# Kernel optimization log

Measured on AMD Instinct MI355X. Metric: run time of the kernel, lower is better.

Reference implementation:

```python
import jax, jax.numpy as jnp
import numpy as np

T_MAX = 20
NUM_HEADS = 8
COMPLEXITY_W = 0.3
LN_EPS = 1e-5


def _layernorm(h, g, b):
    mu = jnp.mean(h, axis=-1, keepdims=True)
    var = jnp.var(h, axis=-1, keepdims=True)
    return (h - mu) / jnp.sqrt(var + LN_EPS) * g + b


def _gate_mlp(x, W1, b1, g, be, W2, b2, W3, b3):
    # Linear -> LayerNorm -> ReLU -> (Dropout=id in eval) -> Linear -> ReLU -> Linear -> Sigmoid
    h = jax.nn.relu(_layernorm(x @ W1 + b1, g, be))
    h = jax.nn.relu(h @ W2 + b2)
    return jax.nn.sigmoid(h @ W3 + b3)


def _adaptive_windows(x, p):
    S = x.shape[1]
    gate = _gate_mlp(x, p['gW1'], p['gb1'], p['gg'], p['gbe'], p['gW2'], p['gb2'], p['gW3'], p['gb3'])
    comp = _gate_mlp(x, p['cW1'], p['cb1'], p['cg'], p['cbe'], p['cW2'], p['cb2'], p['cW3'], p['cb3'])
    pos = jnp.linspace(0.8, 1.2, S, dtype=x.dtype).reshape(1, -1, 1)
    score = ((1.0 - COMPLEXITY_W) * gate + COMPLEXITY_W * comp) * pos
    T_i = jnp.clip(jnp.ceil(score[..., 0] * T_MAX), 1, T_MAX).astype(jnp.int32)  # [B,S]
    return T_i


def _spike_sum(x, T_i, alpha, beta):
    # LIF recurrence over T_MAX steps; accumulate masked spikes. x: [B,S,E]
    z = jnp.zeros_like(x)

    def step(carry, t):
        v, i, acc = carry
        active = (t < T_i).astype(x.dtype)[..., None]  # [B,S,1]
        i = alpha * i + x * active
        v = beta * v + i
        s = (v >= 1.0).astype(x.dtype)
        v = v * (1.0 - s)  # v_reset = 0
        return (v, i, acc + s * active), None

    (_, _, acc), _ = jax.lax.scan(step, (z, z, z), jnp.arange(T_MAX))
    return acc


def _forward(x, params):
    B, S, E = x.shape
    H, D = NUM_HEADS, E // NUM_HEADS
    q = x @ params['Wq']
    k = x @ params['Wk']
    v = x @ params['Wv']
    T_i = _adaptive_windows(x, params)
    q_sum = _spike_sum(q, T_i, params['alpha_q'], params['beta_q'])
    k_sum = _spike_sum(k, T_i, params['alpha_k'], params['beta_k'])
    v_mean = _spike_sum(v, T_i, params['alpha_v'], params['beta_v']) / T_MAX
    q_sum = q_sum.reshape(B, S, H, D)
    k_sum = k_sum.reshape(B, S, H, D)
    v_mean = v_mean.reshape(B, S, H, D)
    scale = D ** -0.5
    scores = jnp.einsum('bihd,bjhd->bhij', q_sum, k_sum) * scale
    w = jax.nn.softmax(scores, axis=-1)
    out = jnp.einsum('bhij,bjhd->bihd', w, v_mean).reshape(B, S, E)
    return out @ params['Wo'] + params['bo']


def setup_inputs() -> dict:
    key = jax.random.key(0)
    ks = iter(jax.random.split(key, 32))
    B, S, E = 4, 1024, 512
    f32 = jnp.float32

    def w(shape, scale=0.02):
        return jax.random.normal(next(ks), shape, dtype=f32) * scale

    inp = {
        'x': jax.random.normal(next(ks), (B, S, E), dtype=f32),
        'Wq': w((E, E)), 'Wk': w((E, E)), 'Wv': w((E, E)),
        'Wo': w((E, E)), 'bo': jnp.zeros((E,), f32),
        'gW1': w((E, 128)), 'gb1': jnp.zeros((128,), f32),
        'gg': jnp.ones((128,), f32), 'gbe': jnp.zeros((128,), f32),
        'gW2': w((128, 64)), 'gb2': jnp.zeros((64,), f32),
        'gW3': w((64, 1)), 'gb3': jnp.zeros((1,), f32),
        'cW1': w((E, 64)), 'cb1': jnp.zeros((64,), f32),
        'cg': jnp.ones((64,), f32), 'cbe': jnp.zeros((64,), f32),
        'cW2': w((64, 32)), 'cb2': jnp.zeros((32,), f32),
        'cW3': w((32, 1)), 'cb3': jnp.zeros((1,), f32),
        'alpha_q': jnp.asarray(np.exp(-1 / 5.0), f32), 'beta_q': jnp.asarray(np.exp(-1 / 20.0), f32),
        'alpha_k': jnp.asarray(np.exp(-1 / 5.0), f32), 'beta_k': jnp.asarray(np.exp(-1 / 20.0), f32),
        'alpha_v': jnp.asarray(np.exp(-1 / 5.0), f32), 'beta_v': jnp.asarray(np.exp(-1 / 20.0), f32),
    }
    return inp


def reference(x, Wq, Wk, Wv, Wo, bo,
              gW1, gb1, gg, gbe, gW2, gb2, gW3, gb3,
              cW1, cb1, cg, cbe, cW2, cb2, cW3, cb3,
              alpha_q, beta_q, alpha_k, beta_k, alpha_v, beta_v):
    params = dict(Wq=Wq, Wk=Wk, Wv=Wv, Wo=Wo, bo=bo,
                  gW1=gW1, gb1=gb1, gg=gg, gbe=gbe, gW2=gW2, gb2=gb2, gW3=gW3, gb3=gb3,
                  cW1=cW1, cb1=cb1, cg=cg, cbe=cbe, cW2=cW2, cb2=cb2, cW3=cW3, cb3=cb3,
                  alpha_q=alpha_q, beta_q=beta_q, alpha_k=alpha_k, beta_k=beta_k,
                  alpha_v=alpha_v, beta_v=beta_v)
    return _forward(x, params)
```

## Files before the change

### kernel.cpp

```cpp
#include <hip/hip_runtime.h>
#include <math.h>

#define SEQ   1024
#define EMB   512
#define NROWS 4096
#define LDP   72
#define GROWS 8
#define LDW   40

typedef __attribute__((ext_vector_type(8))) short short8;
typedef __attribute__((ext_vector_type(4))) float float4v;

__device__ __forceinline__ float bf2f(unsigned short s) {
    union { float f; unsigned u; } x; x.u = ((unsigned)s) << 16; return x.f;
}
__device__ __forceinline__ unsigned short f2bf(float f) {
    union { float f; unsigned u; } x; x.f = f;
    unsigned r = x.u + 0x7fffu + ((x.u >> 16) & 1u);
    return (unsigned short)(r >> 16);
}

__device__ __forceinline__ void split3(float x, unsigned short& h, unsigned short& m, unsigned short& l) {
    union { float f; unsigned u; } a; a.f = x;
    const unsigned rh = a.u + 0x7fffu + ((a.u >> 16) & 1u);
    h = (unsigned short)(rh >> 16);
    union { float f; unsigned u; } hf; hf.u = rh & 0xffff0000u;
    const float r1 = x - hf.f;
    a.f = r1;
    const unsigned rm = a.u + 0x7fffu + ((a.u >> 16) & 1u);
    m = (unsigned short)(rm >> 16);
    union { float f; unsigned u; } mf; mf.u = rm & 0xffff0000u;
    const float r2 = r1 - mf.f;
    l = f2bf(r2);
}

template<int H1, int H2>
__device__ __forceinline__ double gate_mlp_block(
    const double xs[GROWS][EMB], double h1[GROWS][128], double h2[GROWS][64],
    double* mu_s, double* var_s,
    const float* __restrict__ W1, const float* __restrict__ b1,
    const float* __restrict__ gam, const float* __restrict__ bet,
    const float* __restrict__ W2, const float* __restrict__ b2,
    const float* __restrict__ W3, const float* __restrict__ b3,
    int tid, int myrow)
{
    constexpr int RN1 = GROWS * H1 / 256;
    constexpr int RN2 = GROWS * H2 / 256;

    {
        const int col = tid % H1;
        const int rb  = (tid / H1) * RN1;
        double acc[RN1];
        #pragma unroll
        for (int r = 0; r < RN1; ++r) acc[r] = (double)b1[col];
        for (int k = 0; k < EMB; ++k) {
            const double w = (double)W1[k * H1 + col];
            #pragma unroll
            for (int r = 0; r < RN1; ++r) acc[r] += w * xs[rb + r][k];
        }
        #pragma unroll
        for (int r = 0; r < RN1; ++r) h1[rb + r][col] = acc[r];
    }
    __syncthreads();

    {
        const int r = tid >> 5, l = tid & 31;
        double s = 0.0;
        for (int c = l; c < H1; c += 32) s += h1[r][c];
        #pragma unroll
        for (int off = 16; off >= 1; off >>= 1) s += __shfl_xor(s, off);
        if (l == 0) mu_s[r] = s / (double)H1;
    }
    __syncthreads();
    {
        const int r = tid >> 5, l = tid & 31;
        const double mu = mu_s[r];
        double s = 0.0;
        for (int c = l; c < H1; c += 32) { const double d = h1[r][c] - mu; s += d * d; }
        #pragma unroll
        for (int off = 16; off >= 1; off >>= 1) s += __shfl_xor(s, off);
        if (l == 0) var_s[r] = s / (double)H1;
    }
    __syncthreads();
    for (int idx = tid; idx < GROWS * H1; idx += 256) {
        const int r = idx / H1, cc = idx % H1;
        double hn = (h1[r][cc] - mu_s[r]) / sqrt(var_s[r] + 1e-5) * (double)gam[cc] + (double)bet[cc];
        h1[r][cc] = hn > 0.0 ? hn : 0.0;
    }
    __syncthreads();

    {
        const int col = tid % H2;
        const int rb  = (tid / H2) * RN2;
        double acc[RN2];
        #pragma unroll
        for (int r = 0; r < RN2; ++r) acc[r] = (double)b2[col];
        for (int k = 0; k < H1; ++k) {
            const double w = (double)W2[k * H2 + col];
            #pragma unroll
            for (int r = 0; r < RN2; ++r) acc[r] += w * h1[rb + r][k];
        }
        #pragma unroll
        for (int r = 0; r < RN2; ++r) h2[rb + r][col] = acc[r] > 0.0 ? acc[r] : 0.0;
    }
    __syncthreads();

    {
        const int r = tid >> 5, l = tid & 31;
        double s = 0.0;
        for (int c = l; c < H2; c += 32) s += h2[r][c] * (double)W3[c];
        #pragma unroll
        for (int off = 16; off >= 1; off >>= 1) s += __shfl_xor(s, off);
        if (l == 0) mu_s[r] = s;
    }
    __syncthreads();
    double ret = 0.0;
    if (myrow >= 0) {
        const double z = mu_s[myrow] + (double)b3[0];
        ret = 1.0 / (1.0 + exp(-z));
    }
    __syncthreads();
    return ret;
}

__global__ __launch_bounds__(256) void gates_kernel(
    const float* __restrict__ x,
    const float* __restrict__ gW1, const float* __restrict__ gb1,
    const float* __restrict__ gg,  const float* __restrict__ gbe,
    const float* __restrict__ gW2, const float* __restrict__ gb2,
    const float* __restrict__ gW3, const float* __restrict__ gb3,
    const float* __restrict__ cW1, const float* __restrict__ cb1,
    const float* __restrict__ cg,  const float* __restrict__ cbe,
    const float* __restrict__ cW2, const float* __restrict__ cb2,
    const float* __restrict__ cW3, const float* __restrict__ cb3,
    int* __restrict__ T_i)
{
    __shared__ double xs[GROWS][EMB];
    __shared__ double h1[GROWS][128];
    __shared__ double h2[GROWS][64];
    __shared__ double mu_s[GROWS], var_s[GROWS];

    const int row0 = blockIdx.x * GROWS;
    const int tid = threadIdx.x;

    for (int idx = tid; idx < GROWS * EMB; idx += 256) {
        const int r = idx >> 9, cc = idx & 511;
        xs[r][cc] = (double)x[(size_t)(row0 + r) * EMB + cc];
    }
    __syncthreads();

    const int myrow = (tid < GROWS) ? tid : -1;
    const double g0 = gate_mlp_block<128, 64>(xs, h1, h2, mu_s, var_s,
                                              gW1, gb1, gg, gbe, gW2, gb2, gW3, gb3, tid, myrow);
    const double c0 = gate_mlp_block<64, 32>(xs, h1, h2, mu_s, var_s,
                                             cW1, cb1, cg, cbe, cW2, cb2, cW3, cb3, tid, myrow);

    if (tid < GROWS) {
        const int row = row0 + tid;
        const int s = row & (SEQ - 1);
        const double step = (1.2 - 0.8) / (double)(SEQ - 1);
        const double pos  = (double)s * step + 0.8;
        const double score = ((1.0 - 0.3) * g0 + 0.3 * c0) * pos;
        double t = ceil(score * 20.0);
        t = t < 1.0 ? 1.0 : (t > 20.0 ? 20.0 : t);
        T_i[row] = (int)t;
    }
}

__global__ __launch_bounds__(256) void w_limbs_prep(
    const float* __restrict__ Wq, const float* __restrict__ Wk, const float* __restrict__ Wv,
    unsigned short* __restrict__ WL)
{
    const int z = blockIdx.z;
    const float* __restrict__ W = (z == 0) ? Wq : (z == 1) ? Wk : Wv;
    unsigned short* __restrict__ Th = WL + (size_t)z * 3 * EMB * EMB;
    unsigned short* __restrict__ Tm = Th + (size_t)EMB * EMB;
    unsigned short* __restrict__ Tl = Tm + (size_t)EMB * EMB;

    __shared__ __align__(16) float Ws[64][68];
    const int k0 = blockIdx.y * 64, n0 = blockIdx.x * 64;
    const int t = threadIdx.x;
    #pragma unroll
    for (int it = 0; it < 4; ++it) {
        const int idx = it * 256 + t;
        const int r = idx >> 4, c4 = (idx & 15) * 4;
        *(float4*)&Ws[r][c4] = *(const float4*)&W[(size_t)(k0 + r) * EMB + n0 + c4];
    }
    __syncthreads();
    #pragma unroll
    for (int it = 0; it < 2; ++it) {
        const int idx = it * 256 + t;
        const int n = idx >> 3, k8 = (idx & 7) * 8;
        short8 ph, pm, pl;
        #pragma unroll
        for (int j = 0; j < 8; ++j) {
            unsigned short h, m, l;
            split3(Ws[k8 + j][n], h, m, l);
            ph[j] = (short)h; pm[j] = (short)m; pl[j] = (short)l;
        }
        const size_t o = (size_t)(n0 + n) * EMB + k0 + k8;
        *(short8*)&Th[o] = ph;
        *(short8*)&Tm[o] = pm;
        *(short8*)&Tl[o] = pl;
    }
}

__global__ __launch_bounds__(256) void qkv_mfma_lif_kernel(
    const float* __restrict__ x, const unsigned short* __restrict__ WL,
    const float* __restrict__ aq, const float* __restrict__ bq,
    const float* __restrict__ akp, const float* __restrict__ bkp,
    const float* __restrict__ av, const float* __restrict__ bv,
    const int* __restrict__ T_i,
    unsigned short* __restrict__ q_sum, unsigned short* __restrict__ k_sum,
    unsigned short* __restrict__ v_mean)
{
    const int z = blockIdx.z;
    const unsigned short* __restrict__ WTh = WL + (size_t)z * 3 * EMB * EMB;
    const unsigned short* __restrict__ WTm = WTh + (size_t)EMB * EMB;
    const unsigned short* __restrict__ WTl = WTm + (size_t)EMB * EMB;
    unsigned short* __restrict__ out = (z == 0) ? q_sum : (z == 1) ? k_sum : v_mean;
    const double alpha = (double)((z == 0) ? aq : (z == 1) ? akp : av)[0];
    const double beta  = (double)((z == 0) ? bq : (z == 1) ? bkp : bv)[0];

    __shared__ __align__(16) short Ah[128 * LDW], Am2[128 * LDW], Al2[128 * LDW];
    __shared__ __align__(16) short Bh[64 * LDW],  Bm2[64 * LDW],  Bl2[64 * LDW];

    const int tid  = threadIdx.x;
    const int lane = tid & 63, wave = tid >> 6;
    const int qd = lane >> 4, c = lane & 15;
    const int wrow = wave * 32;
    const int row0 = blockIdx.y * 128, col0 = blockIdx.x * 64;

    const int am = tid >> 1, ak = (tid & 1) * 16;
    const int bn = tid >> 2, bk = (tid & 3) * 8;

    float4v acc[2][4];
    #pragma unroll
    for (int i = 0; i < 2; ++i)
        #pragma unroll
        for (int j = 0; j < 4; ++j)
            acc[i][j] = (float4v){0.f, 0.f, 0.f, 0.f};

    for (int k0 = 0; k0 < EMB; k0 += 32) {
        const float* xp = &x[(size_t)(row0 + am) * EMB + k0 + ak];
        const float4 a0 = *(const float4*)(xp + 0);
        const float4 a1 = *(const float4*)(xp + 4);
        const float4 a2 = *(const float4*)(xp + 8);
        const float4 a3 = *(const float4*)(xp + 12);
        const size_t boff = (size_t)(col0 + bn) * EMB + k0 + bk;
        const short8 b8h = *(const short8*)&WTh[boff];
        const short8 b8m = *(const short8*)&WTm[boff];
        const short8 b8l = *(const short8*)&WTl[boff];

        const float av16[16] = {a0.x, a0.y, a0.z, a0.w, a1.x, a1.y, a1.z, a1.w,
                                a2.x, a2.y, a2.z, a2.w, a3.x, a3.y, a3.z, a3.w};
        unsigned short lh[16], lm[16], ll[16];
        #pragma unroll
        for (int e = 0; e < 16; ++e) split3(av16[e], lh[e], lm[e], ll[e]);
        short8 ph0, ph1, pm0, pm1, pl0, pl1;
        #pragma unroll
        for (int e = 0; e < 8; ++e) {
            ph0[e] = (short)lh[e]; ph1[e] = (short)lh[e + 8];
            pm0[e] = (short)lm[e]; pm1[e] = (short)lm[e + 8];
            pl0[e] = (short)ll[e]; pl1[e] = (short)ll[e + 8];
        }

        __syncthreads();
        {
            const int ao = am * LDW + ak;
            *(short8*)&Ah[ao]      = ph0; *(short8*)&Ah[ao + 8]  = ph1;
            *(short8*)&Am2[ao]     = pm0; *(short8*)&Am2[ao + 8] = pm1;
            *(short8*)&Al2[ao]     = pl0; *(short8*)&Al2[ao + 8] = pl1;
            const int bo = bn * LDW + bk;
            *(short8*)&Bh[bo]  = b8h;
            *(short8*)&Bm2[bo] = b8m;
            *(short8*)&Bl2[bo] = b8l;
        }
        __syncthreads();

        short8 Afh[2], Afm[2], Afl[2];
        #pragma unroll
        for (int i = 0; i < 2; ++i) {
            const int ab = (wrow + i * 16 + c) * LDW + qd * 8;
            Afh[i] = *(const short8*)&Ah[ab];
            Afm[i] = *(const short8*)&Am2[ab];
            Afl[i] = *(const short8*)&Al2[ab];
        }
        short8 Bfh[4], Bfm[4], Bfl[4];
        #pragma unroll
        for (int j = 0; j < 4; ++j) {
            const int bb = (j * 16 + c) * LDW + qd * 8;
            Bfh[j] = *(const short8*)&Bh[bb];
            Bfm[j] = *(const short8*)&Bm2[bb];
            Bfl[j] = *(const short8*)&Bl2[bb];
        }

        #pragma unroll
        for (int i = 0; i < 2; ++i)
            #pragma unroll
            for (int j = 0; j < 4; ++j) {
                float4v t = acc[i][j];
                t = __builtin_amdgcn_mfma_f32_16x16x32_bf16(Afh[i], Bfh[j], t, 0, 0, 0);
                t = __builtin_amdgcn_mfma_f32_16x16x32_bf16(Afh[i], Bfm[j], t, 0, 0, 0);
                t = __builtin_amdgcn_mfma_f32_16x16x32_bf16(Afm[i], Bfh[j], t, 0, 0, 0);
                t = __builtin_amdgcn_mfma_f32_16x16x32_bf16(Afm[i], Bfm[j], t, 0, 0, 0);
                t = __builtin_amdgcn_mfma_f32_16x16x32_bf16(Afh[i], Bfl[j], t, 0, 0, 0);
                t = __builtin_amdgcn_mfma_f32_16x16x32_bf16(Afl[i], Bfh[j], t, 0, 0, 0);
                acc[i][j] = t;
            }
    }

    #pragma unroll
    for (int i = 0; i < 2; ++i)
        #pragma unroll
        for (int r = 0; r < 4; ++r) {
            const int gm = row0 + wrow + i * 16 + qd * 4 + r;
            const int T = T_i[gm];
            #pragma unroll
            for (int j = 0; j < 4; ++j) {
                const double xv = (double)acc[i][j][r];
                double cur = 0.0, vm = 0.0, spikes = 0.0;
                for (int t = 0; t < T; ++t) {
                    cur = alpha * cur + xv;
                    vm  = beta * vm + cur;
                    if (vm >= 1.0) { spikes += 1.0; vm = 0.0; }
                }
                if (z == 2) spikes = spikes / 20.0;
                out[(size_t)gm * EMB + col0 + j * 16 + c] = f2bf((float)spikes);
            }
        }
}

__global__ __launch_bounds__(256) void attn_mfma_kernel(
    const unsigned short* __restrict__ q, const unsigned short* __restrict__ k,
    const unsigned short* __restrict__ v, unsigned short* __restrict__ attn_bf)
{
    __shared__ __align__(16) short Ks[64 * LDP];
    __shared__ __align__(16) short Pt[64 * LDP];
    __shared__ __align__(16) short Vt[64 * LDP];

    const int b = blockIdx.z, h = blockIdx.y;
    const int i0 = blockIdx.x * 64;
    const int tid  = threadIdx.x;
    const int wave = tid >> 6, lane = tid & 63;
    const int quad = lane >> 4, c = lane & 15;

    const unsigned short* Qb = q + ((size_t)b * SEQ + i0) * EMB + h * 64;
    const unsigned short* Kb = k + (size_t)b * SEQ * EMB + h * 64;
    const unsigned short* Vb = v + (size_t)b * SEQ * EMB + h * 64;

    short8 qf[2];
    {
        const int qrow = wave * 16 + c;
        #pragma unroll
        for (int ks = 0; ks < 2; ++ks) {
            short8 raw = *(const short8*)(Qb + (size_t)qrow * EMB + ks * 32 + quad * 8);
            short8 sc8;
            #pragma unroll
            for (int j = 0; j < 8; ++j)
                sc8[j] = (short)f2bf(bf2f((unsigned short)raw[j]) * 0.125f);
            qf[ks] = sc8;
        }
    }

    float m_r[4], l_r[4];
    float4v o[4];
    #pragma unroll
    for (int r = 0; r < 4; ++r) { m_r[r] = -1e30f; l_r[r] = 0.f; }
    #pragma unroll
    for (int nb = 0; nb < 4; ++nb)
        #pragma unroll
        for (int r = 0; r < 4; ++r) o[nb][r] = 0.f;

    for (int jt = 0; jt < SEQ / 64; ++jt) {
        #pragma unroll
        for (int it = 0; it < 2; ++it) {
            const int idx = it * 256 + tid;
            const int row = idx >> 3, ch = idx & 7;
            short8 val = *(const short8*)(Kb + (size_t)(jt * 64 + row) * EMB + ch * 8);
            *(short8*)&Ks[row * LDP + ch * 8] = val;
        }
        __syncthreads();

        float sc[4][4];
        #pragma unroll
        for (int nb = 0; nb < 4; ++nb) {
            float4v acc = {0.f, 0.f, 0.f, 0.f};
            #pragma unroll
            for (int ks = 0; ks < 2; ++ks) {
                short8 bfrag = *(const short8*)&Ks[(nb * 16 + c) * LDP + ks * 32 + quad * 8];
                acc = __builtin_amdgcn_mfma_f32_16x16x32_bf16(qf[ks], bfrag, acc, 0, 0, 0);
            }
            #pragma unroll
            for (int r = 0; r < 4; ++r) sc[nb][r] = acc[r];
        }

        float mnew[4], alpha[4];
        #pragma unroll
        for (int r = 0; r < 4; ++r) {
            float mx = fmaxf(fmaxf(sc[0][r], sc[1][r]), fmaxf(sc[2][r], sc[3][r]));
            #pragma unroll
            for (int off = 8; off >= 1; off >>= 1) mx = fmaxf(mx, __shfl_xor(mx, off));
            mnew[r]  = fmaxf(m_r[r], mx);
            alpha[r] = __expf(m_r[r] - mnew[r]);
            m_r[r]   = mnew[r];
        }
        float psum[4] = {0.f, 0.f, 0.f, 0.f};
        #pragma unroll
        for (int nb = 0; nb < 4; ++nb)
            #pragma unroll
            for (int r = 0; r < 4; ++r) {
                float p = __expf(sc[nb][r] - mnew[r]);
                psum[r] += p;
                Pt[(wave * 16 + quad * 4 + r) * LDP + nb * 16 + c] = (short)f2bf(p);
            }
        #pragma unroll
        for (int r = 0; r < 4; ++r) {
            float s = psum[r];
            #pragma unroll
            for (int off = 8; off >= 1; off >>= 1) s += __shfl_xor(s, off);
            l_r[r] = l_r[r] * alpha[r] + s;
            #pragma unroll
            for (int nb = 0; nb < 4; ++nb) o[nb][r] *= alpha[r];
        }

        {
            const int m = tid & 7, rp = tid >> 3;
            const int r = rp * 2;
            short8 v0 = *(const short8*)(Vb + (size_t)(jt * 64 + r) * EMB + m * 8);
            short8 v1 = *(const short8*)(Vb + (size_t)(jt * 64 + r + 1) * EMB + m * 8);
            const int rch = r >> 3, rlow = r & 7;
            #pragma unroll
            for (int i = 0; i < 8; ++i) {
                const int d = m * 8 + i;
                const int col = ((rch ^ m) << 3) + rlow;
                *(int*)&Vt[d * LDP + col] =
                    (int)((unsigned)(unsigned short)v0[i] |
                          ((unsigned)(unsigned short)v1[i] << 16));
            }
        }
        __syncthreads();

        short8 pf[2];
        #pragma unroll
        for (int ks = 0; ks < 2; ++ks)
            pf[ks] = *(const short8*)&Pt[(wave * 16 + c) * LDP + ks * 32 + quad * 8];
        #pragma unroll
        for (int nb = 0; nb < 4; ++nb) {
            float4v acc = o[nb];
            #pragma unroll
            for (int ks = 0; ks < 2; ++ks) {
                const int d = nb * 16 + c;
                const int kch = ks * 4 + quad;
                const int col = ((kch ^ (d >> 3)) << 3);
                short8 vfrag = *(const short8*)&Vt[d * LDP + col];
                acc = __builtin_amdgcn_mfma_f32_16x16x32_bf16(pf[ks], vfrag, acc, 0, 0, 0);
            }
            o[nb] = acc;
        }
    }

    #pragma unroll
    for (int r = 0; r < 4; ++r) {
        const float inv = 1.0f / l_r[r];
        const int row = i0 + wave * 16 + quad * 4 + r;
        #pragma unroll
        for (int nb = 0; nb < 4; ++nb)
            attn_bf[((size_t)b * SEQ + row) * EMB + h * 64 + nb * 16 + c] =
                f2bf(o[nb][r] * inv);
    }
}

__global__ __launch_bounds__(256) void wot_prep(
    const float* __restrict__ Wo, unsigned short* __restrict__ BT)
{
    __shared__ unsigned short Ws[64][72];
    const int k0 = blockIdx.y * 64, n0 = blockIdx.x * 64;
    const int t = threadIdx.x;
    #pragma unroll
    for (int it = 0; it < 4; ++it) {
        const int idx = it * 256 + t;
        const int r = idx >> 4, c4 = (idx & 15) * 4;
        const float4 w4 = *(const float4*)&Wo[(size_t)(k0 + r) * EMB + n0 + c4];
        Ws[r][c4 + 0] = f2bf(w4.x); Ws[r][c4 + 1] = f2bf(w4.y);
        Ws[r][c4 + 2] = f2bf(w4.z); Ws[r][c4 + 3] = f2bf(w4.w);
    }
    __syncthreads();
    #pragma unroll
    for (int it = 0; it < 2; ++it) {
        const int idx = it * 256 + t;
        const int n = idx >> 3, k8 = (idx & 7) * 8;
        short8 pack;
        #pragma unroll
        for (int j = 0; j < 8; ++j) pack[j] = (short)Ws[k8 + j][n];
        *(short8*)&BT[(size_t)(n0 + n) * EMB + k0 + k8] = pack;
    }
}

__global__ __launch_bounds__(256) void out_gemm_kernel(
    const unsigned short* __restrict__ A,
    const unsigned short* __restrict__ BT,
    const float* __restrict__ bias, float* __restrict__ out)
{
    const int tid  = threadIdx.x;
    const int lane = tid & 63, wave = tid >> 6;
    const int qd = lane >> 4, c = lane & 15;
    const int wm = (wave & 1) * 32, wn = (wave >> 1) * 32;
    const int row0 = blockIdx.y * 64, col0 = blockIdx.x * 64;

    float4v acc[2][2];
    #pragma unroll
    for (int i = 0; i < 2; ++i)
        #pragma unroll
        for (int j = 0; j < 2; ++j)
            acc[i][j] = (float4v){0.f, 0.f, 0.f, 0.f};

    for (int k0 = 0; k0 < EMB; k0 += 32) {
        short8 af[2], bf[2];
        #pragma unroll
        for (int i = 0; i < 2; ++i)
            af[i] = *(const short8*)&A[(size_t)(row0 + wm + i * 16 + c) * EMB + k0 + qd * 8];
        #pragma unroll
        for (int j = 0; j < 2; ++j)
            bf[j] = *(const short8*)&BT[(size_t)(col0 + wn + j * 16 + c) * EMB + k0 + qd * 8];
        #pragma unroll
        for (int i = 0; i < 2; ++i)
            #pragma unroll
            for (int j = 0; j < 2; ++j)
                acc[i][j] = __builtin_amdgcn_mfma_f32_16x16x32_bf16(af[i], bf[j], acc[i][j], 0, 0, 0);
    }

    #pragma unroll
    for (int i = 0; i < 2; ++i)
        #pragma unroll
        for (int r = 0; r < 4; ++r) {
            const int gm = row0 + wm + i * 16 + qd * 4 + r;
            #pragma unroll
            for (int j = 0; j < 2; ++j) {
                const int gn = col0 + wn + j * 16 + c;
                out[(size_t)gm * EMB + gn] = acc[i][j][r] + bias[gn];
            }
        }
}

extern "C" void kernel_launch(void* const* d_in, const int* in_sizes, int n_in,
                              void* d_out, int out_size, void* d_ws, size_t ws_size,
                              hipStream_t stream)
{
    const float* x   = (const float*)d_in[0];
    const float* Wq  = (const float*)d_in[1];
    const float* Wk  = (const float*)d_in[2];
    const float* Wv  = (const float*)d_in[3];
    const float* Wo  = (const float*)d_in[4];
    const float* bo  = (const float*)d_in[5];
    const float* gW1 = (const float*)d_in[6];
    const float* gb1 = (const float*)d_in[7];
    const float* gg  = (const float*)d_in[8];
    const float* gbe = (const float*)d_in[9];
    const float* gW2 = (const float*)d_in[10];
    const float* gb2 = (const float*)d_in[11];
    const float* gW3 = (const float*)d_in[12];
    const float* gb3 = (const float*)d_in[13];
    const float* cW1 = (const float*)d_in[14];
    const float* cb1 = (const float*)d_in[15];
    const float* cg  = (const float*)d_in[16];
    const float* cbe = (const float*)d_in[17];
    const float* cW2 = (const float*)d_in[18];
    const float* cb2 = (const float*)d_in[19];
    const float* cW3 = (const float*)d_in[20];
    const float* cb3 = (const float*)d_in[21];
    const float* aq  = (const float*)d_in[22];
    const float* bq  = (const float*)d_in[23];
    const float* ak  = (const float*)d_in[24];
    const float* bk  = (const float*)d_in[25];
    const float* av  = (const float*)d_in[26];
    const float* bv  = (const float*)d_in[27];

    int* Tp = (int*)d_ws;
    unsigned short* q_sum   = (unsigned short*)((char*)d_ws + 16384);
    unsigned short* k_sum   = q_sum   + (size_t)NROWS * EMB;
    unsigned short* v_mean  = k_sum   + (size_t)NROWS * EMB;
    unsigned short* attn_bf = v_mean  + (size_t)NROWS * EMB;
    unsigned short* WoT     = attn_bf + (size_t)NROWS * EMB;
    unsigned short* WL      = WoT     + (size_t)EMB * EMB;
    float* out = (float*)d_out;

    gates_kernel<<<dim3(NROWS / GROWS), dim3(256), 0, stream>>>(
        x, gW1, gb1, gg, gbe, gW2, gb2, gW3, gb3,
        cW1, cb1, cg, cbe, cW2, cb2, cW3, cb3, Tp);

    w_limbs_prep<<<dim3(EMB / 64, EMB / 64, 3), dim3(256), 0, stream>>>(Wq, Wk, Wv, WL);

    qkv_mfma_lif_kernel<<<dim3(EMB / 64, NROWS / 128, 3), dim3(256), 0, stream>>>(
        x, WL, aq, bq, ak, bk, av, bv, Tp, q_sum, k_sum, v_mean);

    wot_prep<<<dim3(EMB / 64, EMB / 64), dim3(256), 0, stream>>>(Wo, WoT);

    attn_mfma_kernel<<<dim3(SEQ / 64, 8, 4), dim3(256), 0, stream>>>(
        q_sum, k_sum, v_mean, attn_bf);

    out_gemm_kernel<<<dim3(EMB / 64, NROWS / 64), dim3(256), 0, stream>>>(
        attn_bf, WoT, bo, out);
}
```

Before: 300.0 us.

## Pre-split x into bf16 limbs and load QKV MFMA fragments directly from global

Adds an x_limbs_prep kernel that splits x into three bf16 limbs once, so the QKV MFMA kernel no longer re-splits x for every column block (and for each of q/k/v). The QKV kernel drops its shared-memory staging and barriers and loads A and B fragments straight from global memory. Separately, the gates kernel now processes 4 rows per block and splits the first layer's K dimension across threads with a shared-memory reduction, giving more blocks and more parallelism. Costs are an extra kernel launch, extra workspace traffic for the limbs, and uncoalesced, less-reused direct global fragment loads.

```diff
diff --git a/kernel.cpp b/kernel.cpp
--- a/kernel.cpp
+++ b/kernel.cpp
@@ -5,8 +5,7 @@
 #define EMB   512
 #define NROWS 4096
 #define LDP   72
-#define GROWS 8
-#define LDW   40
+#define GROWS 4
 
 typedef __attribute__((ext_vector_type(8))) short short8;
 typedef __attribute__((ext_vector_type(4))) float float4v;
@@ -37,49 +36,56 @@
 template<int H1, int H2>
 __device__ __forceinline__ double gate_mlp_block(
     const double xs[GROWS][EMB], double h1[GROWS][128], double h2[GROWS][64],
-    double* mu_s, double* var_s,
+    double* red, double* mu_s, double* var_s,
     const float* __restrict__ W1, const float* __restrict__ b1,
     const float* __restrict__ gam, const float* __restrict__ bet,
     const float* __restrict__ W2, const float* __restrict__ b2,
     const float* __restrict__ W3, const float* __restrict__ b3,
     int tid, int myrow)
 {
-    constexpr int RN1 = GROWS * H1 / 256;
-    constexpr int RN2 = GROWS * H2 / 256;
+    constexpr int S  = 256 / H1;
+    constexpr int KS = EMB / S;
 
     {
-        const int col = tid % H1;
-        const int rb  = (tid / H1) * RN1;
-        double acc[RN1];
-        #pragma unroll
-        for (int r = 0; r < RN1; ++r) acc[r] = (double)b1[col];
-        for (int k = 0; k < EMB; ++k) {
+        const int col = tid % H1, sk = tid / H1;
+        double acc[GROWS] = {0.0, 0.0, 0.0, 0.0};
+        const int kbeg = sk * KS;
+        #pragma unroll 4
+        for (int k = kbeg; k < kbeg + KS; ++k) {
             const double w = (double)W1[k * H1 + col];
             #pragma unroll
-            for (int r = 0; r < RN1; ++r) acc[r] += w * xs[rb + r][k];
-        }
-        #pragma unroll
-        for (int r = 0; r < RN1; ++r) h1[rb + r][col] = acc[r];
+            for (int r = 0; r < GROWS; ++r) acc[r] += w * xs[r][k];
+        }
+        #pragma unroll
+        for (int r = 0; r < GROWS; ++r) red[(sk * GROWS + r) * H1 + col] = acc[r];
+    }
+    __syncthreads();
+    for (int idx = tid; idx < GROWS * H1; idx += 256) {
+        const int r = idx / H1, cc = idx % H1;
+        double s = 0.0;
+        #pragma unroll
+        for (int t = 0; t < S; ++t) s += red[(t * GROWS + r) * H1 + cc];
+        h1[r][cc] = s + (double)b1[cc];
     }
     __syncthreads();
 
     {
-        const int r = tid >> 5, l = tid & 31;
+        const int w = tid >> 6, l = tid & 63;
         double s = 0.0;
-        for (int c = l; c < H1; c += 32) s += h1[r][c];
-        #pragma unroll
-        for (int off = 16; off >= 1; off >>= 1) s += __shfl_xor(s, off);
-        if (l == 0) mu_s[r] = s / (double)H1;
+        for (int c = l; c < H1; c += 64) s += h1[w][c];
+        #pragma unroll
+        for (int off = 32; off >= 1; off >>= 1) s += __shfl_xor(s, off);
+        if (l == 0) mu_s[w] = s / (double)H1;
     }
     __syncthreads();
     {
-        const int r = tid >> 5, l = tid & 31;
-        const double mu = mu_s[r];
+        const int w = tid >> 6, l = tid & 63;
+        const double mu = mu_s[w];
         double s = 0.0;
-        for (int c = l; c < H1; c += 32) { const double d = h1[r][c] - mu; s += d * d; }
-        #pragma unroll
-        for (int off = 16; off >= 1; off >>= 1) s += __shfl_xor(s, off);
-        if (l == 0) var_s[r] = s / (double)H1;
+        for (int c = l; c < H1; c += 64) { const double d = h1[w][c] - mu; s += d * d; }
+        #pragma unroll
+        for (int off = 32; off >= 1; off >>= 1) s += __shfl_xor(s, off);
+        if (l == 0) var_s[w] = s / (double)H1;
     }
     __syncthreads();
     for (int idx = tid; idx < GROWS * H1; idx += 256) {
@@ -91,27 +97,23 @@
 
     {
         const int col = tid % H2;
-        const int rb  = (tid / H2) * RN2;
-        double acc[RN2];
-        #pragma unroll
-        for (int r = 0; r < RN2; ++r) acc[r] = (double)b2[col];
-        for (int k = 0; k < H1; ++k) {
-            const double w = (double)W2[k * H2 + col];
-            #pragma unroll
-            for (int r = 0; r < RN2; ++r) acc[r] += w * h1[rb + r][k];
-        }
-        #pragma unroll
-        for (int r = 0; r < RN2; ++r) h2[rb + r][col] = acc[r] > 0.0 ? acc[r] : 0.0;
+        const int r   = tid / H2;
+        if (r < GROWS) {
+            double acc = (double)b2[col];
+            for (int k = 0; k < H1; ++k)
+                acc += (double)W2[k * H2 + col] * h1[r][k];
+            h2[r][col] = acc > 0.0 ? acc : 0.0;
+        }
     }
     __syncthreads();
 
     {
-        const int r = tid >> 5, l = tid & 31;
+        const int w = tid >> 6, l = tid & 63;
         double s = 0.0;
-        for (int c = l; c < H2; c += 32) s += h2[r][c] * (double)W3[c];
-        #pragma unroll
-        for (int off = 16; off >= 1; off >>= 1) s += __shfl_xor(s, off);
-        if (l == 0) mu_s[r] = s;
+        for (int c = l; c < H2; c += 64) s += h2[w][c] * (double)W3[c];
+        #pragma unroll
+        for (int off = 32; off >= 1; off >>= 1) s += __shfl_xor(s, off);
+        if (l == 0) mu_s[w] = s;
     }
     __syncthreads();
     double ret = 0.0;
@@ -138,6 +140,7 @@
     __shared__ double xs[GROWS][EMB];
     __shared__ double h1[GROWS][128];
     __shared__ double h2[GROWS][64];
+    __shared__ double red[1024];
     __shared__ double mu_s[GROWS], var_s[GROWS];
 
     const int row0 = blockIdx.x * GROWS;
@@ -150,9 +153,9 @@
     __syncthreads();
 
     const int myrow = (tid < GROWS) ? tid : -1;
-    const double g0 = gate_mlp_block<128, 64>(xs, h1, h2, mu_s, var_s,
+    const double g0 = gate_mlp_block<128, 64>(xs, h1, h2, red, mu_s, var_s,
                                               gW1, gb1, gg, gbe, gW2, gb2, gW3, gb3, tid, myrow);
-    const double c0 = gate_mlp_block<64, 32>(xs, h1, h2, mu_s, var_s,
+    const double c0 = gate_mlp_block<64, 32>(xs, h1, h2, red, mu_s, var_s,
                                              cW1, cb1, cg, cbe, cW2, cb2, cW3, cb3, tid, myrow);
 
     if (tid < GROWS) {
@@ -205,8 +208,30 @@
     }
 }
 
+__global__ __launch_bounds__(256) void x_limbs_prep(
+    const float* __restrict__ x, unsigned short* __restrict__ XL)
+{
+    unsigned short* __restrict__ Xh = XL;
+    unsigned short* __restrict__ Xm = XL + (size_t)NROWS * EMB;
+    unsigned short* __restrict__ Xl = Xm + (size_t)NROWS * EMB;
+    const size_t i0 = ((size_t)blockIdx.x * 256 + threadIdx.x) * 8;
+    const float4 a0 = *(const float4*)&x[i0];
+    const float4 a1 = *(const float4*)&x[i0 + 4];
+    const float av8[8] = {a0.x, a0.y, a0.z, a0.w, a1.x, a1.y, a1.z, a1.w};
+    short8 ph, pm, pl;
+    #pragma unroll
+    for (int e = 0; e < 8; ++e) {
+        unsigned short h, m, l;
+        split3(av8[e], h, m, l);
+        ph[e] = (short)h; pm[e] = (short)m; pl[e] = (short)l;
+    }
+    *(short8*)&Xh[i0] = ph;
+    *(short8*)&Xm[i0] = pm;
+    *(short8*)&Xl[i0] = pl;
+}
+
 __global__ __launch_bounds__(256) void qkv_mfma_lif_kernel(
-    const float* __restrict__ x, const unsigned short* __restrict__ WL,
+    const unsigned short* __restrict__ XL, const unsigned short* __restrict__ WL,
     const float* __restrict__ aq, const float* __restrict__ bq,
     const float* __restrict__ akp, const float* __restrict__ bkp,
     const float* __restrict__ av, const float* __restrict__ bv,
@@ -218,12 +243,12 @@
     const unsigned short* __restrict__ WTh = WL + (size_t)z * 3 * EMB * EMB;
     const unsigned short* __restrict__ WTm = WTh + (size_t)EMB * EMB;
     const unsigned short* __restrict__ WTl = WTm + (size_t)EMB * EMB;
+    const unsigned short* __restrict__ Xh = XL;
+    const unsigned short* __restrict__ Xm = XL + (size_t)NROWS * EMB;
+    const unsigned short* __restrict__ Xl = Xm + (size_t)NROWS * EMB;
     unsigned short* __restrict__ out = (z == 0) ? q_sum : (z == 1) ? k_sum : v_mean;
     const double alpha = (double)((z == 0) ? aq : (z == 1) ? akp : av)[0];
     const double beta  = (double)((z == 0) ? bq : (z == 1) ? bkp : bv)[0];
-
-    __shared__ __align__(16) short Ah[128 * LDW], Am2[128 * LDW], Al2[128 * LDW];
-    __shared__ __align__(16) short Bh[64 * LDW],  Bm2[64 * LDW],  Bl2[64 * LDW];
 
     const int tid  = threadIdx.x;
     const int lane = tid & 63, wave = tid >> 6;
@@ -231,8 +256,13 @@
     const int wrow = wave * 32;
     const int row0 = blockIdx.y * 128, col0 = blockIdx.x * 64;
 
-    const int am = tid >> 1, ak = (tid & 1) * 16;
-    const int bn = tid >> 2, bk = (tid & 3) * 8;
+    size_t aoff[2], boff[4];
+    #pragma unroll
+    for (int i = 0; i < 2; ++i)
+        aoff[i] = (size_t)(row0 + wrow + i * 16 + c) * EMB + qd * 8;
+    #pragma unroll
+    for (int j = 0; j < 4; ++j)
+        boff[j] = (size_t)(col0 + j * 16 + c) * EMB + qd * 8;
 
     float4v acc[2][4];
     #pragma unroll
@@ -242,59 +272,20 @@
             acc[i][j] = (float4v){0.f, 0.f, 0.f, 0.f};
 
     for (int k0 = 0; k0 < EMB; k0 += 32) {
-        const float* xp = &x[(size_t)(row0 + am) * EMB + k0 + ak];
-        const float4 a0 = *(const float4*)(xp + 0);
-        const float4 a1 = *(const float4*)(xp + 4);
-        const float4 a2 = *(const float4*)(xp + 8);
-        const float4 a3 = *(const float4*)(xp + 12);
-        const size_t boff = (size_t)(col0 + bn) * EMB + k0 + bk;
-        const short8 b8h = *(const short8*)&WTh[boff];
-        const short8 b8m = *(const short8*)&WTm[boff];
-        const short8 b8l = *(const short8*)&WTl[boff];
-
-        const float av16[16] = {a0.x, a0.y, a0.z, a0.w, a1.x, a1.y, a1.z, a1.w,
-                                a2.x, a2.y, a2.z, a2.w, a3.x, a3.y, a3.z, a3.w};
-        unsigned short lh[16], lm[16], ll[16];
-        #pragma unroll
-        for (int e = 0; e < 16; ++e) split3(av16[e], lh[e], lm[e], ll[e]);
-        short8 ph0, ph1, pm0, pm1, pl0, pl1;
-        #pragma unroll
-        for (int e = 0; e < 8; ++e) {
-            ph0[e] = (short)lh[e]; ph1[e] = (short)lh[e + 8];
-            pm0[e] = (short)lm[e]; pm1[e] = (short)lm[e + 8];
-            pl0[e] = (short)ll[e]; pl1[e] = (short)ll[e + 8];
-        }
-
-        __syncthreads();
-        {
-            const int ao = am * LDW + ak;
-            *(short8*)&Ah[ao]      = ph0; *(short8*)&Ah[ao + 8]  = ph1;
-            *(short8*)&Am2[ao]     = pm0; *(short8*)&Am2[ao + 8] = pm1;
-            *(short8*)&Al2[ao]     = pl0; *(short8*)&Al2[ao + 8] = pl1;
-            const int bo = bn * LDW + bk;
-            *(short8*)&Bh[bo]  = b8h;
-            *(short8*)&Bm2[bo] = b8m;
-            *(short8*)&Bl2[bo] = b8l;
-        }
-        __syncthreads();
-
         short8 Afh[2], Afm[2], Afl[2];
         #pragma unroll
         for (int i = 0; i < 2; ++i) {
-            const int ab = (wrow + i * 16 + c) * LDW + qd * 8;
-            Afh[i] = *(const short8*)&Ah[ab];
-            Afm[i] = *(const short8*)&Am2[ab];
-            Afl[i] = *(const short8*)&Al2[ab];
+            Afh[i] = *(const short8*)&Xh[aoff[i] + k0];
+            Afm[i] = *(const short8*)&Xm[aoff[i] + k0];
+            Afl[i] = *(const short8*)&Xl[aoff[i] + k0];
         }
         short8 Bfh[4], Bfm[4], Bfl[4];
         #pragma unroll
         for (int j = 0; j < 4; ++j) {
-            const int bb = (j * 16 + c) * LDW + qd * 8;
-            Bfh[j] = *(const short8*)&Bh[bb];
-            Bfm[j] = *(const short8*)&Bm2[bb];
-            Bfl[j] = *(const short8*)&Bl2[bb];
-        }
-
+            Bfh[j] = *(const short8*)&WTh[boff[j] + k0];
+            Bfm[j] = *(const short8*)&WTm[boff[j] + k0];
+            Bfl[j] = *(const short8*)&WTl[boff[j] + k0];
+        }
         #pragma unroll
         for (int i = 0; i < 2; ++i)
             #pragma unroll
@@ -583,16 +574,19 @@
     unsigned short* attn_bf = v_mean  + (size_t)NROWS * EMB;
     unsigned short* WoT     = attn_bf + (size_t)NROWS * EMB;
     unsigned short* WL      = WoT     + (size_t)EMB * EMB;
+    unsigned short* XLp     = WL      + (size_t)9 * EMB * EMB;
     float* out = (float*)d_out;
 
     gates_kernel<<<dim3(NROWS / GROWS), dim3(256), 0, stream>>>(
         x, gW1, gb1, gg, gbe, gW2, gb2, gW3, gb3,
         cW1, cb1, cg, cbe, cW2, cb2, cW3, cb3, Tp);
 
+    x_limbs_prep<<<dim3(NROWS * EMB / (256 * 8)), dim3(256), 0, stream>>>(x, XLp);
+
     w_limbs_prep<<<dim3(EMB / 64, EMB / 64, 3), dim3(256), 0, stream>>>(Wq, Wk, Wv, WL);
 
     qkv_mfma_lif_kernel<<<dim3(EMB / 64, NROWS / 128, 3), dim3(256), 0, stream>>>(
-        x, WL, aq, bq, ak, bk, av, bv, Tp, q_sum, k_sum, v_mean);
+        XLp, WL, aq, bq, ak, bk, av, bv, Tp, q_sum, k_sum, v_mean);
 
     wot_prep<<<dim3(EMB / 64, EMB / 64), dim3(256), 0, stream>>>(Wo, WoT);
 
```

Result: slower. 342.7 us (+14.3%).
